# Kernel optimization log

Hardware: AMD Instinct MI355X
Metric: run time of the kernel (lower is better)

Reference implementation:

```python
import jax, jax.numpy as jnp
import numpy as np

POOLSCALE = 4  # HSA: avg-pool kernel/stride = (scale, scale*4)

def _avg_pool(x, kh, kw):
    # kernel == stride and dims divisible -> exact reshape-mean pooling
    B, C, H, W = x.shape
    return x.reshape(B, C, H // kh, kh, W // kw, kw).mean(axis=(3, 5))

def setup_inputs() -> dict:
    key = jax.random.key(0)
    k1, k2, k3 = jax.random.split(key, 3)
    shape = (4, 64, 192, 192)
    return {
        "K": jax.random.normal(k1, shape, dtype=jnp.float32),
        "Q": jax.random.normal(k2, shape, dtype=jnp.float32),
        "V": jax.random.normal(k3, shape, dtype=jnp.float32),
    }

def reference(K, Q, V):
    B, C, H, W = Q.shape
    kh, kw = POOLSCALE, POOLSCALE * 4
    Qp = Q.reshape(B, C, H * W).transpose(0, 2, 1)          # [B, HW, C]
    Kp = _avg_pool(K, kh, kw)                               # [B, C, h, w]
    Kp = Kp.reshape(B, C, -1)                               # [B, C, hw_p]
    Vp = _avg_pool(V, kh, kw).reshape(B, C, -1)             # [B, C, hw_p]
    scores = jnp.einsum('bnc,bcm->bnm', Qp, Kp)             # [B, HW, hw_p]
    attn = jax.nn.softmax(scores, axis=1)                   # softmax over query dim (dim=1), as in torch code
    out = jnp.einsum('bcm,bnm->bcn', Vp, attn)              # V_pie @ attn^T -> [B, C, HW]
    return out.reshape(B, C, H, W)
```

## Files before the change

### kernel.cpp

```cpp
#include <hip/hip_runtime.h>
#include <stdint.h>

#define BB 4
#define CC 64
#define HH 192
#define WW 192
#define HWN (HH*WW)
#define KH 4
#define KW 16
#define PW (WW/KW)
#define MP ((HH/KH)*(WW/KW))
#define MITER (MP/64)
#define NCHUNK (HWN/256)
#define NBTOT (HWN/32)
#define SCALE_W 65536.0f
#define INV_SCALE (1.0f/65536.0f)

typedef _Float16 half8 __attribute__((ext_vector_type(8)));
typedef _Float16 half4 __attribute__((ext_vector_type(4)));
typedef float floatx4 __attribute__((ext_vector_type(4)));

static __device__ __forceinline__ void gload16(const void* g, void* l) {
  __builtin_amdgcn_global_load_lds((const __attribute__((address_space(1))) void*)g,
                                   (__attribute__((address_space(3))) void*)l, 16, 0, 0);
}
#define WAITCNT_VM(N) asm volatile("s_waitcnt vmcnt(" #N ")" ::: "memory")
#define WAITCNT_LGKM0 asm volatile("s_waitcnt lgkmcnt(0)" ::: "memory")


__global__ __launch_bounds__(256) void pool_kernel(
    const float* __restrict__ Kin, const float* __restrict__ Vin,
    _Float16* __restrict__ kptF, float* __restrict__ vp) {
  int t = blockIdx.x * 256 + threadIdx.x;
  const int total = BB * CC * MP;
  bool isV = t >= total;
  int idx = isV ? t - total : t;
  int m = idx % MP;
  int c = (idx / MP) % CC;
  int b = idx / (MP * CC);
  int mh = m / PW, mw = m % PW;
  const float* src = (isV ? Vin : Kin) + (((b * CC + c) * HH + mh * KH) * WW + mw * KW);
  float s = 0.f;
#pragma unroll
  for (int r = 0; r < KH; ++r) {
    const float4* row = (const float4*)(src + r * WW);
#pragma unroll
    for (int j = 0; j < KW / 4; ++j) {
      float4 v = row[j];
      s += v.x + v.y + v.z + v.w;
    }
  }
  s *= (1.0f / (KH * KW));
  if (isV) {
    vp[(b * CC + c) * MP + m] = s;
  } else {
    int mi = m >> 6, mloc = m & 63, l15 = mloc >> 2, mf = mloc & 3;
    int ks = c >> 5, lhi = (c >> 3) & 3, e = c & 7;
    int lane = lhi * 16 + l15;
    kptF[(((((b * MITER + mi) * 4 + mf) * 2 + ks)) * 64 + lane) * 8 + e] = (_Float16)s;
  }
}

__global__ __launch_bounds__(256) void qprep_kernel(
    const float* __restrict__ Q, _Float16* __restrict__ qF) {
  int t = blockIdx.x * 256 + threadIdx.x;
  int chunk = t >> 6;
  int lane = t & 63;
  int nf = chunk & 1;
  int ks = (chunk >> 1) & 1;
  int idx = chunk >> 2;
  int nb = idx % NBTOT;
  int b = idx / NBTOT;
  int c0 = ks * 32 + (lane >> 4) * 8;
  int n = nb * 32 + nf * 16 + (lane & 15);
  const float* Qb = Q + (b * CC + c0) * HWN + n;
  half8 h;
#pragma unroll
  for (int e = 0; e < 8; ++e) h[e] = (_Float16)Qb[e * HWN];
  *(half8*)(qF + chunk * 512 + lane * 8) = h;
}

__global__ __launch_bounds__(512) void colsum_qf_kernel(
    const _Float16* __restrict__ qF, const _Float16* __restrict__ kptF,
    float* __restrict__ part) {
  int tid = threadIdx.x;
  int lane = tid & 63;
  int l15 = lane & 15;
  int u = blockIdx.x * 8 + (tid >> 6);
  int mi = u % 9;
  int v = u / 9;
  int b = v / NCHUNK;
  int nc = v % NCHUNK;

  const _Float16* kb = kptF + b * MITER * 8 * 512;
  half8 bfr[4][2];
#pragma unroll
  for (int mf = 0; mf < 4; ++mf)
#pragma unroll
    for (int ks = 0; ks < 2; ++ks)
      bfr[mf][ks] = *(const half8*)(kb + ((mi * 4 + mf) * 2 + ks) * 512 + lane * 8);

  floatx4 zero = {0.f, 0.f, 0.f, 0.f};
  float s0 = 0.f, s1 = 0.f, s2 = 0.f, s3 = 0.f;

#pragma unroll
  for (int it = 0; it < 8; ++it) {
    int nb = nc * 8 + it;
    const _Float16* qc = qF + (size_t)((b * NBTOT + nb) * 4) * 512 + lane * 8;
    half8 af[2][2];
#pragma unroll
    for (int ks = 0; ks < 2; ++ks)
#pragma unroll
      for (int nf = 0; nf < 2; ++nf)
        af[nf][ks] = *(const half8*)(qc + (ks * 2 + nf) * 512);

    floatx4 sacc[2][4];
#pragma unroll
    for (int nf = 0; nf < 2; ++nf)
#pragma unroll
      for (int mf = 0; mf < 4; ++mf) sacc[nf][mf] = zero;
    __builtin_amdgcn_s_setprio(1);
#pragma unroll
    for (int ks = 0; ks < 2; ++ks)
#pragma unroll
      for (int nf = 0; nf < 2; ++nf)
#pragma unroll
        for (int mf = 0; mf < 4; ++mf)
          sacc[nf][mf] = __builtin_amdgcn_mfma_f32_16x16x32_f16(
              af[nf][ks], bfr[mf][ks], sacc[nf][mf], 0, 0, 0);
    __builtin_amdgcn_s_setprio(0);

#pragma unroll
    for (int nf = 0; nf < 2; ++nf)
#pragma unroll
      for (int r = 0; r < 4; ++r) {
        s0 += __expf(sacc[nf][0][r]);
        s1 += __expf(sacc[nf][1][r]);
        s2 += __expf(sacc[nf][2][r]);
        s3 += __expf(sacc[nf][3][r]);
      }
  }

  s0 += __shfl_xor(s0, 16); s0 += __shfl_xor(s0, 32);
  s1 += __shfl_xor(s1, 16); s1 += __shfl_xor(s1, 32);
  s2 += __shfl_xor(s2, 16); s2 += __shfl_xor(s2, 32);
  s3 += __shfl_xor(s3, 16); s3 += __shfl_xor(s3, 32);
  if (lane < 16) {
    float* p = part + (b * NCHUNK + nc) * MP + mi * 64 + l15 * 4;
    p[0] = s0; p[1] = s1; p[2] = s2; p[3] = s3;
  }
}

__global__ __launch_bounds__(576) void colsum_fb_kernel(
    const float* __restrict__ Q, const _Float16* __restrict__ kptF,
    float* __restrict__ part) {
  int b = blockIdx.y;
  int n0 = blockIdx.x * 256;
  int tid = threadIdx.x;
  int wv = tid / 64;
  int lane = tid & 63;
  int l15 = lane & 15, lhi = lane >> 4;

  const _Float16* kb = kptF + b * MITER * 8 * 512;
  half8 bfr[4][2];
#pragma unroll
  for (int mf = 0; mf < 4; ++mf)
#pragma unroll
    for (int ks = 0; ks < 2; ++ks)
      bfr[mf][ks] = *(const half8*)(kb + ((wv * 4 + mf) * 2 + ks) * 512 + lane * 8);

  const float* Qb = Q + b * CC * HWN;
  floatx4 zero = {0.f, 0.f, 0.f, 0.f};
  float s0 = 0.f, s1 = 0.f, s2 = 0.f, s3 = 0.f;

#pragma unroll
  for (int it = 0; it < 8; ++it) {
    int nr = n0 + it * 32 + l15;
    half8 af[2][2];
#pragma unroll
    for (int nf = 0; nf < 2; ++nf)
#pragma unroll
      for (int ks = 0; ks < 2; ++ks)
#pragma unroll
        for (int e = 0; e < 8; ++e)
          af[nf][ks][e] = (_Float16)Qb[(ks * 32 + lhi * 8 + e) * HWN + nr + nf * 16];

    floatx4 sacc[2][4];
#pragma unroll
    for (int nf = 0; nf < 2; ++nf)
#pragma unroll
      for (int mf = 0; mf < 4; ++mf) sacc[nf][mf] = zero;
    __builtin_amdgcn_s_setprio(1);
#pragma unroll
    for (int ks = 0; ks < 2; ++ks)
#pragma unroll
      for (int nf = 0; nf < 2; ++nf)
#pragma unroll
        for (int mf = 0; mf < 4; ++mf)
          sacc[nf][mf] = __builtin_amdgcn_mfma_f32_16x16x32_f16(
              af[nf][ks], bfr[mf][ks], sacc[nf][mf], 0, 0, 0);
    __builtin_amdgcn_s_setprio(0);

#pragma unroll
    for (int nf = 0; nf < 2; ++nf)
#pragma unroll
      for (int r = 0; r < 4; ++r) {
        s0 += __expf(sacc[nf][0][r]);
        s1 += __expf(sacc[nf][1][r]);
        s2 += __expf(sacc[nf][2][r]);
        s3 += __expf(sacc[nf][3][r]);
      }
  }

  s0 += __shfl_xor(s0, 16); s0 += __shfl_xor(s0, 32);
  s1 += __shfl_xor(s1, 16); s1 += __shfl_xor(s1, 32);
  s2 += __shfl_xor(s2, 16); s2 += __shfl_xor(s2, 32);
  s3 += __shfl_xor(s3, 16); s3 += __shfl_xor(s3, 32);
  if (lane < 16) {
    float* p = part + (b * NCHUNK + blockIdx.x) * MP + wv * 64 + l15 * 4;
    p[0] = s0; p[1] = s1; p[2] = s2; p[3] = s3;
  }
}

__global__ __launch_bounds__(256) void colsum_reduce_kernel(
    const float* __restrict__ part, float* __restrict__ colsum) {
  int t = blockIdx.x * 256 + threadIdx.x;
  int m = t % MP;
  int b = t / MP;
  const float* p = part + b * NCHUNK * MP + m;
  float a0 = 0.f, a1 = 0.f, a2 = 0.f, a3 = 0.f;
#pragma unroll 4
  for (int nc = 0; nc < NCHUNK; nc += 4) {
    a0 += p[(nc + 0) * MP];
    a1 += p[(nc + 1) * MP];
    a2 += p[(nc + 2) * MP];
    a3 += p[(nc + 3) * MP];
  }
  colsum[t] = (a0 + a1) + (a2 + a3);
}

__global__ __launch_bounds__(256) void wprep_kernel(
    const float* __restrict__ vp, const float* __restrict__ colsum,
    _Float16* __restrict__ wqF) {
  int t = blockIdx.x * 256 + threadIdx.x;
  int m = t % MP;
  int c = (t / MP) % CC;
  int b = t / (CC * MP);
  float w = vp[t] / colsum[b * MP + m] * SCALE_W;
  int cf = c >> 4, l15 = c & 15;
  int mi = m >> 6, mloc = m & 63;
  int ks = mloc >> 5, lhi = (mloc >> 3) & 3, e = mloc & 7;
  int lane = lhi * 16 + l15;
  wqF[((((b * MITER + mi) * 4 + cf) * 2 + ks) * 64 + lane) * 8 + e] = (_Float16)w;
}

__global__ __launch_bounds__(256) void attn_qf_kernel(
    const _Float16* __restrict__ qF, const _Float16* __restrict__ kptF,
    const _Float16* __restrict__ wqF, float* __restrict__ out) {
  __shared__ char lds[2 * 16384 + 4 * 4096];
  char* stg = lds;
  int b = blockIdx.y;
  int tid = threadIdx.x;
  int wv = tid >> 6;
  int lane = tid & 63;
  int l15 = lane & 15, lhi = lane >> 4;
  char* eb = lds + 32768 + wv * 4096;

  const _Float16* kb = kptF + b * MITER * 8 * 512;
  const _Float16* wb = wqF + b * MITER * 8 * 512;

#define STAGE_Q(tt, ss)                                                        \
  {                                                                            \
    int q0_ = wv * 4;                                                          \
    _Pragma("unroll") for (int j_ = 0; j_ < 4; ++j_) {                         \
      int q_ = q0_ + j_;                                                       \
      const _Float16* sp_ = (q_ < 8 ? kb + (tt) * 4096 + q_ * 512              \
                                    : wb + (tt) * 4096 + (q_ - 8) * 512) +     \
                            lane * 8;                                          \
      gload16(sp_, stg + (ss) * 16384 + q_ * 1024);                            \
    }                                                                          \
  }

  STAGE_Q(0, 0);

  int nb = blockIdx.x * 4 + wv;
  const _Float16* qc = qF + (size_t)((b * NBTOT + nb) * 4) * 512 + lane * 8;
  half8 afrag[2][2];
#pragma unroll
  for (int ks = 0; ks < 2; ++ks)
#pragma unroll
    for (int nf = 0; nf < 2; ++nf)
      afrag[nf][ks] = *(const half8*)(qc + (ks * 2 + nf) * 512);

  floatx4 zero = {0.f, 0.f, 0.f, 0.f};
  floatx4 oacc[4][2];
#pragma unroll
  for (int cf = 0; cf < 4; ++cf)
#pragma unroll
    for (int nf = 0; nf < 2; ++nf) oacc[cf][nf] = zero;

#pragma unroll
  for (int mi = 0; mi < MITER; ++mi) {
    const int sc = mi & 1;
    WAITCNT_LGKM0;
    WAITCNT_VM(0);
    __builtin_amdgcn_sched_barrier(0);
    __builtin_amdgcn_s_barrier();
    if (mi + 1 < MITER) STAGE_Q(mi + 1, sc ^ 1);

    half8 bfr[4][2];
#pragma unroll
    for (int mf = 0; mf < 4; ++mf)
#pragma unroll
      for (int ks = 0; ks < 2; ++ks)
        bfr[mf][ks] = *(const half8*)(stg + sc * 16384 + (mf * 2 + ks) * 1024 + lane * 16);
    half8 wfr[4][2];
#pragma unroll
    for (int cf = 0; cf < 4; ++cf)
#pragma unroll
      for (int ks = 0; ks < 2; ++ks)
        wfr[cf][ks] = *(const half8*)(stg + sc * 16384 + 8192 + (cf * 2 + ks) * 1024 + lane * 16);

    floatx4 sacc[2][4];
#pragma unroll
    for (int nf = 0; nf < 2; ++nf)
#pragma unroll
      for (int mf = 0; mf < 4; ++mf) sacc[nf][mf] = zero;
    __builtin_amdgcn_s_setprio(1);
#pragma unroll
    for (int ks = 0; ks < 2; ++ks)
#pragma unroll
      for (int nf = 0; nf < 2; ++nf)
#pragma unroll
        for (int mf = 0; mf < 4; ++mf)
          sacc[nf][mf] = __builtin_amdgcn_mfma_f32_16x16x32_f16(
              afrag[nf][ks], bfr[mf][ks], sacc[nf][mf], 0, 0, 0);
    __builtin_amdgcn_s_setprio(0);

#pragma unroll
    for (int nf = 0; nf < 2; ++nf)
#pragma unroll
      for (int r = 0; r < 4; ++r) {
        int nl = nf * 16 + lhi * 4 + r;
        half4 h;
#pragma unroll
        for (int mf = 0; mf < 4; ++mf) h[mf] = (_Float16)__expf(sacc[nf][mf][r]);
        int byte = nl * 128 + ((((l15 >> 1) ^ (nl & 7))) << 4) + ((l15 & 1) << 3);
        *(half4*)(eb + byte) = h;
      }

    half8 ef[2][2];
#pragma unroll
    for (int nf = 0; nf < 2; ++nf)
#pragma unroll
      for (int ks = 0; ks < 2; ++ks) {
        int nl = nf * 16 + l15;
        int slot = (ks * 4 + lhi) ^ (nl & 7);
        ef[nf][ks] = *(const half8*)(eb + nl * 128 + (slot << 4));
      }
    __builtin_amdgcn_s_setprio(1);
#pragma unroll
    for (int ks = 0; ks < 2; ++ks)
#pragma unroll
      for (int cf = 0; cf < 4; ++cf)
#pragma unroll
        for (int nf = 0; nf < 2; ++nf)
          oacc[cf][nf] = __builtin_amdgcn_mfma_f32_16x16x32_f16(
              wfr[cf][ks], ef[nf][ks], oacc[cf][nf], 0, 0, 0);
    __builtin_amdgcn_s_setprio(0);
  }

  float* ob = out + b * CC * HWN;
#pragma unroll
  for (int cf = 0; cf < 4; ++cf)
#pragma unroll
    for (int nf = 0; nf < 2; ++nf)
#pragma unroll
      for (int r = 0; r < 4; ++r) {
        int c = cf * 16 + lhi * 4 + r;
        int n = nb * 32 + nf * 16 + l15;
        ob[c * HWN + n] = oacc[cf][nf][r] * INV_SCALE;
      }
}

__global__ __launch_bounds__(256, 2) void attn_main_kernel(
    const float* __restrict__ Q, const _Float16* __restrict__ kptF,
    const _Float16* __restrict__ wqF, float* __restrict__ out) {
  __shared__ char lds[3 * 16384 + 4 * 4096];
  char* stg = lds;
  int b = blockIdx.y;
  int n0 = blockIdx.x * 128;
  int tid = threadIdx.x;
  int wv = tid >> 6;
  int lane = tid & 63;
  int l15 = lane & 15, lhi = lane >> 4;
  char* eb = lds + 49152 + wv * 4096;

  const _Float16* kb = kptF + b * MITER * 8 * 512;
  const _Float16* wb = wqF + b * MITER * 8 * 512;

#define STAGE_A(tt, ss)                                                        \
  {                                                                            \
    int q0_ = wv * 4;                                                          \
    _Pragma("unroll") for (int j_ = 0; j_ < 4; ++j_) {                         \
      int q_ = q0_ + j_;                                                       \
      const _Float16* sp_ = (q_ < 8 ? kb + (tt) * 4096 + q_ * 512              \
                                    : wb + (tt) * 4096 + (q_ - 8) * 512) +     \
                            lane * 8;                                          \
      gload16(sp_, stg + (ss) * 16384 + q_ * 1024);                            \
    }                                                                          \
  }

  STAGE_A(0, 0);
  STAGE_A(1, 1);

  const float* Qb = Q + b * CC * HWN;
  int nrow = n0 + wv * 32 + l15;
  half8 afrag[2][2];
#pragma unroll
  for (int nf = 0; nf < 2; ++nf)
#pragma unroll
    for (int ks = 0; ks < 2; ++ks)
#pragma unroll
      for (int e = 0; e < 8; ++e)
        afrag[nf][ks][e] = (_Float16)Qb[(ks * 32 + lhi * 8 + e) * HWN + nrow + nf * 16];

  floatx4 zero = {0.f, 0.f, 0.f, 0.f};
  floatx4 oacc[4][2];
#pragma unroll
  for (int cf = 0; cf < 4; ++cf)
#pragma unroll
    for (int nf = 0; nf < 2; ++nf) oacc[cf][nf] = zero;

  WAITCNT_VM(4);
  __builtin_amdgcn_sched_barrier(0);
  __builtin_amdgcn_s_barrier();

#pragma unroll
  for (int mi = 0; mi < MITER; ++mi) {
    const int sc = mi % 3;
    const int spv = (mi + 2) % 3;

    if (mi >= 1) {
      if (mi <= 7) { WAITCNT_VM(4); } else { WAITCNT_VM(0); }
      __builtin_amdgcn_sched_barrier(0);
      __builtin_amdgcn_s_barrier();
    }

    half8 bfr[4][2];
#pragma unroll
    for (int mf = 0; mf < 4; ++mf)
#pragma unroll
      for (int ks = 0; ks < 2; ++ks)
        bfr[mf][ks] = *(const half8*)(stg + sc * 16384 + (mf * 2 + ks) * 1024 + lane * 16);
    half8 wfr[4][2];
    half8 ef[2][2];
    if (mi >= 1) {
#pragma unroll
      for (int cf = 0; cf < 4; ++cf)
#pragma unroll
        for (int ks = 0; ks < 2; ++ks)
          wfr[cf][ks] = *(const half8*)(stg + spv * 16384 + 8192 + (cf * 2 + ks) * 1024 + lane * 16);
#pragma unroll
      for (int nf = 0; nf < 2; ++nf)
#pragma unroll
        for (int ks = 0; ks < 2; ++ks) {
          int nl = nf * 16 + l15;
          int slot = (ks * 4 + lhi) ^ (nl & 7);
          ef[nf][ks] = *(const half8*)(eb + nl * 128 + (slot << 4));
        }
    }

    WAITCNT_LGKM0;
    __builtin_amdgcn_sched_barrier(0);
    __builtin_amdgcn_s_barrier();

    if (mi + 2 < MITER) STAGE_A(mi + 2, spv);

    floatx4 sacc[2][4];
#pragma unroll
    for (int nf = 0; nf < 2; ++nf)
#pragma unroll
      for (int mf = 0; mf < 4; ++mf) sacc[nf][mf] = zero;
    __builtin_amdgcn_s_setprio(1);
#pragma unroll
    for (int ks = 0; ks < 2; ++ks)
#pragma unroll
      for (int nf = 0; nf < 2; ++nf)
#pragma unroll
        for (int mf = 0; mf < 4; ++mf)
          sacc[nf][mf] = __builtin_amdgcn_mfma_f32_16x16x32_f16(
              afrag[nf][ks], bfr[mf][ks], sacc[nf][mf], 0, 0, 0);
    if (mi >= 1) {
#pragma unroll
      for (int ks = 0; ks < 2; ++ks)
#pragma unroll
        for (int cf = 0; cf < 4; ++cf)
#pragma unroll
          for (int nf = 0; nf < 2; ++nf)
            oacc[cf][nf] = __builtin_amdgcn_mfma_f32_16x16x32_f16(
                wfr[cf][ks], ef[nf][ks], oacc[cf][nf], 0, 0, 0);
    }
    __builtin_amdgcn_s_setprio(0);

#pragma unroll
    for (int nf = 0; nf < 2; ++nf)
#pragma unroll
      for (int r = 0; r < 4; ++r) {
        int nl = nf * 16 + lhi * 4 + r;
        half4 h;
#pragma unroll
        for (int mf = 0; mf < 4; ++mf) h[mf] = (_Float16)__expf(sacc[nf][mf][r]);
        int byte = nl * 128 + ((((l15 >> 1) ^ (nl & 7))) << 4) + ((l15 & 1) << 3);
        *(half4*)(eb + byte) = h;
      }
  }

  {
    half8 wfr[4][2];
#pragma unroll
    for (int cf = 0; cf < 4; ++cf)
#pragma unroll
      for (int ks = 0; ks < 2; ++ks)
        wfr[cf][ks] = *(const half8*)(stg + 2 * 16384 + 8192 + (cf * 2 + ks) * 1024 + lane * 16);
    half8 ef[2][2];
#pragma unroll
    for (int nf = 0; nf < 2; ++nf)
#pragma unroll
      for (int ks = 0; ks < 2; ++ks) {
        int nl = nf * 16 + l15;
        int slot = (ks * 4 + lhi) ^ (nl & 7);
        ef[nf][ks] = *(const half8*)(eb + nl * 128 + (slot << 4));
      }
    __builtin_amdgcn_s_setprio(1);
#pragma unroll
    for (int ks = 0; ks < 2; ++ks)
#pragma unroll
      for (int cf = 0; cf < 4; ++cf)
#pragma unroll
        for (int nf = 0; nf < 2; ++nf)
          oacc[cf][nf] = __builtin_amdgcn_mfma_f32_16x16x32_f16(
              wfr[cf][ks], ef[nf][ks], oacc[cf][nf], 0, 0, 0);
    __builtin_amdgcn_s_setprio(0);
  }

  float* ob = out + b * CC * HWN;
#pragma unroll
  for (int cf = 0; cf < 4; ++cf)
#pragma unroll
    for (int nf = 0; nf < 2; ++nf)
#pragma unroll
      for (int r = 0; r < 4; ++r) {
        int c = cf * 16 + lhi * 4 + r;
        int n = n0 + wv * 32 + nf * 16 + l15;
        ob[c * HWN + n] = oacc[cf][nf][r] * INV_SCALE;
      }
}

extern "C" void kernel_launch(void* const* d_in, const int* in_sizes, int n_in,
                              void* d_out, int out_size, void* d_ws, size_t ws_size,
                              hipStream_t stream) {
  const float* K = (const float*)d_in[0];
  const float* Q = (const float*)d_in[1];
  const float* V = (const float*)d_in[2];
  float* out = (float*)d_out;
  char* ws = (char*)d_ws;
  _Float16* kptF  = (_Float16*)(ws);
  float*    vp    = (float*)(ws + 294912);
  _Float16* wqF   = (_Float16*)(ws + 294912 + 589824);
  float*    colsum = (float*)(ws + 294912 + 589824 + 294912);
  const size_t QF_OFF = 1204224;
  const size_t QF_BYTES = (size_t)BB * NBTOT * 4 * 512 * 2;
  _Float16* qF = (_Float16*)(ws + QF_OFF);
  float* part = out;

  pool_kernel<<<(2 * BB * CC * MP) / 256, 256, 0, stream>>>(K, V, kptF, vp);
  if (ws_size >= QF_OFF + QF_BYTES) {
    qprep_kernel<<<(BB * NBTOT * 4 * 64) / 256, 256, 0, stream>>>(Q, qF);
    colsum_qf_kernel<<<(BB * NCHUNK * 9) / 8, 512, 0, stream>>>(qF, kptF, part);
    colsum_reduce_kernel<<<(BB * MP) / 256, 256, 0, stream>>>(part, colsum);
    wprep_kernel<<<(BB * CC * MP) / 256, 256, 0, stream>>>(vp, colsum, wqF);
    attn_qf_kernel<<<dim3(NBTOT / 4, BB), 256, 0, stream>>>(qF, kptF, wqF, out);
  } else {
    colsum_fb_kernel<<<dim3(NCHUNK, BB), 576, 0, stream>>>(Q, kptF, part);
    colsum_reduce_kernel<<<(BB * MP) / 256, 256, 0, stream>>>(part, colsum);
    wprep_kernel<<<(BB * CC * MP) / 256, 256, 0, stream>>>(vp, colsum, wqF);
    attn_main_kernel<<<dim3(HWN / 128, BB), 256, 0, stream>>>(Q, kptF, wqF, out);
  }
}
```

Measured before the change: 85.55 us.

## Restructure colsum kernel so each wave keeps Q tile and loops over all keys

The column-sum kernel used to give each wave a fixed key block and stream 8 query blocks (256 queries) through it. Now each wave holds a 64-query Q tile in registers and loops over all 9 key blocks, loading K fragments on each pass. Q is read once instead of 9 times, but the partial buffer grows 4x (one slice per 64 queries instead of per 256), so the reduction kernel reads much more data. Part of that cost moves into a larger reduce step.

New measurement: 107.4 us. 1.25x slower.

```diff
diff --git a/kernel.cpp b/kernel.cpp
--- a/kernel.cpp
+++ b/kernel.cpp
@@ -13,6 +13,7 @@
 #define MITER (MP/64)
 #define NCHUNK (HWN/256)
 #define NBTOT (HWN/32)
+#define NUNIT (HWN/64)
 #define SCALE_W 65536.0f
 #define INV_SCALE (1.0f/65536.0f)
 
@@ -80,75 +81,93 @@
   *(half8*)(qF + chunk * 512 + lane * 8) = h;
 }
 
-__global__ __launch_bounds__(512) void colsum_qf_kernel(
+__global__ __launch_bounds__(256) void colsum_qf2_kernel(
     const _Float16* __restrict__ qF, const _Float16* __restrict__ kptF,
     float* __restrict__ part) {
   int tid = threadIdx.x;
   int lane = tid & 63;
   int l15 = lane & 15;
-  int u = blockIdx.x * 8 + (tid >> 6);
-  int mi = u % 9;
-  int v = u / 9;
-  int b = v / NCHUNK;
-  int nc = v % NCHUNK;
+  int u = blockIdx.x * 4 + (tid >> 6);
+  int b = u / NUNIT;
+  int un = u % NUNIT;
+
+  const _Float16* qc = qF + (size_t)((b * NBTOT + un * 2) * 4) * 512 + lane * 8;
+  half8 af[2][2][2];
+#pragma unroll
+  for (int nb = 0; nb < 2; ++nb)
+#pragma unroll
+    for (int ks = 0; ks < 2; ++ks)
+#pragma unroll
+      for (int nf = 0; nf < 2; ++nf)
+        af[nb][nf][ks] = *(const half8*)(qc + (nb * 4 + ks * 2 + nf) * 512);
 
   const _Float16* kb = kptF + b * MITER * 8 * 512;
-  half8 bfr[4][2];
-#pragma unroll
-  for (int mf = 0; mf < 4; ++mf)
-#pragma unroll
-    for (int ks = 0; ks < 2; ++ks)
-      bfr[mf][ks] = *(const half8*)(kb + ((mi * 4 + mf) * 2 + ks) * 512 + lane * 8);
-
   floatx4 zero = {0.f, 0.f, 0.f, 0.f};
-  float s0 = 0.f, s1 = 0.f, s2 = 0.f, s3 = 0.f;
-
-#pragma unroll
-  for (int it = 0; it < 8; ++it) {
-    int nb = nc * 8 + it;
-    const _Float16* qc = qF + (size_t)((b * NBTOT + nb) * 4) * 512 + lane * 8;
-    half8 af[2][2];
-#pragma unroll
-    for (int ks = 0; ks < 2; ++ks)
+  float* pout = part + (size_t)(b * NUNIT + un) * MP;
+
+#pragma unroll
+  for (int mi = 0; mi < MITER; ++mi) {
+    half8 bfr[4][2];
+#pragma unroll
+    for (int mf = 0; mf < 4; ++mf)
+#pragma unroll
+      for (int ks = 0; ks < 2; ++ks)
+        bfr[mf][ks] = *(const half8*)(kb + ((mi * 4 + mf) * 2 + ks) * 512 + lane * 8);
+
+    float s0 = 0.f, s1 = 0.f, s2 = 0.f, s3 = 0.f;
+#pragma unroll
+    for (int nb = 0; nb < 2; ++nb) {
+      floatx4 sacc[2][4];
 #pragma unroll
       for (int nf = 0; nf < 2; ++nf)
-        af[nf][ks] = *(const half8*)(qc + (ks * 2 + nf) * 512);
-
-    floatx4 sacc[2][4];
-#pragma unroll
-    for (int nf = 0; nf < 2; ++nf)
-#pragma unroll
-      for (int mf = 0; mf < 4; ++mf) sacc[nf][mf] = zero;
-    __builtin_amdgcn_s_setprio(1);
-#pragma unroll
-    for (int ks = 0; ks < 2; ++ks)
+#pragma unroll
+        for (int mf = 0; mf < 4; ++mf) sacc[nf][mf] = zero;
+      __builtin_amdgcn_s_setprio(1);
+#pragma unroll
+      for (int ks = 0; ks < 2; ++ks)
+#pragma unroll
+        for (int nf = 0; nf < 2; ++nf)
+#pragma unroll
+          for (int mf = 0; mf < 4; ++mf)
+            sacc[nf][mf] = __builtin_amdgcn_mfma_f32_16x16x32_f16(
+                af[nb][nf][ks], bfr[mf][ks], sacc[nf][mf], 0, 0, 0);
+      __builtin_amdgcn_s_setprio(0);
 #pragma unroll
       for (int nf = 0; nf < 2; ++nf)
 #pragma unroll
-        for (int mf = 0; mf < 4; ++mf)
-          sacc[nf][mf] = __builtin_amdgcn_mfma_f32_16x16x32_f16(
-              af[nf][ks], bfr[mf][ks], sacc[nf][mf], 0, 0, 0);
-    __builtin_amdgcn_s_setprio(0);
-
-#pragma unroll
-    for (int nf = 0; nf < 2; ++nf)
-#pragma unroll
-      for (int r = 0; r < 4; ++r) {
-        s0 += __expf(sacc[nf][0][r]);
-        s1 += __expf(sacc[nf][1][r]);
-        s2 += __expf(sacc[nf][2][r]);
-        s3 += __expf(sacc[nf][3][r]);
-      }
-  }
-
-  s0 += __shfl_xor(s0, 16); s0 += __shfl_xor(s0, 32);
-  s1 += __shfl_xor(s1, 16); s1 += __shfl_xor(s1, 32);
-  s2 += __shfl_xor(s2, 16); s2 += __shfl_xor(s2, 32);
-  s3 += __shfl_xor(s3, 16); s3 += __shfl_xor(s3, 32);
-  if (lane < 16) {
-    float* p = part + (b * NCHUNK + nc) * MP + mi * 64 + l15 * 4;
-    p[0] = s0; p[1] = s1; p[2] = s2; p[3] = s3;
-  }
+        for (int r = 0; r < 4; ++r) {
+          s0 += __expf(sacc[nf][0][r]);
+          s1 += __expf(sacc[nf][1][r]);
+          s2 += __expf(sacc[nf][2][r]);
+          s3 += __expf(sacc[nf][3][r]);
+        }
+    }
+    s0 += __shfl_xor(s0, 16); s0 += __shfl_xor(s0, 32);
+    s1 += __shfl_xor(s1, 16); s1 += __shfl_xor(s1, 32);
+    s2 += __shfl_xor(s2, 16); s2 += __shfl_xor(s2, 32);
+    s3 += __shfl_xor(s3, 16); s3 += __shfl_xor(s3, 32);
+    if (lane < 16) {
+      float* p = pout + mi * 64 + l15 * 4;
+      p[0] = s0; p[1] = s1; p[2] = s2; p[3] = s3;
+    }
+  }
+}
+
+__global__ __launch_bounds__(256) void colsum_reduce2_kernel(
+    const float* __restrict__ part, float* __restrict__ colsum) {
+  int t = blockIdx.x * 256 + threadIdx.x;
+  int m = t % MP;
+  int b = t / MP;
+  const float* p = part + (size_t)b * NUNIT * MP + m;
+  float a0 = 0.f, a1 = 0.f, a2 = 0.f, a3 = 0.f;
+#pragma unroll 4
+  for (int un = 0; un < NUNIT; un += 4) {
+    a0 += p[(size_t)(un + 0) * MP];
+    a1 += p[(size_t)(un + 1) * MP];
+    a2 += p[(size_t)(un + 2) * MP];
+    a3 += p[(size_t)(un + 3) * MP];
+  }
+  colsum[t] = (a0 + a1) + (a2 + a3);
 }
 
 __global__ __launch_bounds__(576) void colsum_fb_kernel(
@@ -222,7 +241,7 @@
   }
 }
 
-__global__ __launch_bounds__(256) void colsum_reduce_kernel(
+__global__ __launch_bounds__(256) void colsum_reduce_fb_kernel(
     const float* __restrict__ part, float* __restrict__ colsum) {
   int t = blockIdx.x * 256 + threadIdx.x;
   int m = t % MP;
@@ -577,13 +596,13 @@
   pool_kernel<<<(2 * BB * CC * MP) / 256, 256, 0, stream>>>(K, V, kptF, vp);
   if (ws_size >= QF_OFF + QF_BYTES) {
     qprep_kernel<<<(BB * NBTOT * 4 * 64) / 256, 256, 0, stream>>>(Q, qF);
-    colsum_qf_kernel<<<(BB * NCHUNK * 9) / 8, 512, 0, stream>>>(qF, kptF, part);
-    colsum_reduce_kernel<<<(BB * MP) / 256, 256, 0, stream>>>(part, colsum);
+    colsum_qf2_kernel<<<(BB * NUNIT) / 4, 256, 0, stream>>>(qF, kptF, part);
+    colsum_reduce2_kernel<<<(BB * MP) / 256, 256, 0, stream>>>(part, colsum);
     wprep_kernel<<<(BB * CC * MP) / 256, 256, 0, stream>>>(vp, colsum, wqF);
     attn_qf_kernel<<<dim3(NBTOT / 4, BB), 256, 0, stream>>>(qF, kptF, wqF, out);
   } else {
     colsum_fb_kernel<<<dim3(NCHUNK, BB), 576, 0, stream>>>(Q, kptF, part);
-    colsum_reduce_kernel<<<(BB * MP) / 256, 256, 0, stream>>>(part, colsum);
+    colsum_reduce_fb_kernel<<<(BB * MP) / 256, 256, 0, stream>>>(part, colsum);
     wprep_kernel<<<(BB * CC * MP) / 256, 256, 0, stream>>>(vp, colsum, wqF);
     attn_main_kernel<<<dim3(HWN / 128, BB), 256, 0, stream>>>(Q, kptF, wqF, out);
   }
```
